# Kernel optimization log

Measured on AMD Instinct MI355X. Metric: run time of the kernel, lower is better.

The kernel has to match this reference:

```python
import jax, jax.numpy as jnp
import numpy as np

SH_C0 = 0.28209479177387814
SH_C1 = 0.4886025119029199
SH_C2 = (1.0925484305920792, -1.0925484305920792, 0.31539156525252005, -1.0925484305920792, 0.5462742152960396)
SH_C3 = (-0.5900435899266435, 2.890611442640554, -0.4570457994644658, 0.3731763325901154, -0.4570457994644658, 1.445305721320277, -0.5900435899266435)

BG = 128  # gaussians per compositing block


def quat_to_rot(q):
    # q: [N,4] normalized quaternion (w,x,y,z) -> [N,3,3]
    w, x, y, z = q[:, 0], q[:, 1], q[:, 2], q[:, 3]
    R = jnp.stack([
        1 - 2 * (y * y + z * z), 2 * (x * y - w * z), 2 * (x * z + w * y),
        2 * (x * y + w * z), 1 - 2 * (x * x + z * z), 2 * (y * z - w * x),
        2 * (x * z - w * y), 2 * (y * z + w * x), 1 - 2 * (x * x + y * y)],
        axis=-1)
    return R.reshape(-1, 3, 3)


def eval_sh(sh, d):
    # sh: [N,16,3] degree-3 SH coeffs; d: [N,3] unit view dirs -> [N,3] rgb
    x, y, z = d[:, 0:1], d[:, 1:2], d[:, 2:3]
    xx, yy, zz = x * x, y * y, z * z
    xy, yz, xz = x * y, y * z, x * z
    res = SH_C0 * sh[:, 0]
    res = res - SH_C1 * y * sh[:, 1] + SH_C1 * z * sh[:, 2] - SH_C1 * x * sh[:, 3]
    res = (res + SH_C2[0] * xy * sh[:, 4] + SH_C2[1] * yz * sh[:, 5]
           + SH_C2[2] * (2 * zz - xx - yy) * sh[:, 6]
           + SH_C2[3] * xz * sh[:, 7] + SH_C2[4] * (xx - yy) * sh[:, 8])
    res = (res + SH_C3[0] * y * (3 * xx - yy) * sh[:, 9] + SH_C3[1] * xy * z * sh[:, 10]
           + SH_C3[2] * y * (4 * zz - xx - yy) * sh[:, 11]
           + SH_C3[3] * z * (2 * zz - 3 * xx - 3 * yy) * sh[:, 12]
           + SH_C3[4] * x * (4 * zz - xx - yy) * sh[:, 13]
           + SH_C3[5] * z * (xx - yy) * sh[:, 14] + SH_C3[6] * x * (xx - 3 * yy) * sh[:, 15])
    return res


def gs_forward(pws, shs, alphas_raw, scales_raw, rots_raw, us, Rcw, tcw, intr, height, width):
    fx, fy, cx, cy = intr[0], intr[1], intr[2], intr[3]
    N = pws.shape[0]
    HW = height * width

    # activations (GSModel.forward)
    alphas = jax.nn.sigmoid(alphas_raw[:, 0])          # [N]
    scales = jnp.exp(scales_raw)                       # [N,3]
    rots = rots_raw / jnp.linalg.norm(rots_raw, axis=1, keepdims=True)

    # gsc.project
    pcs = pws @ Rcw.T + tcw                            # [N,3] camera frame
    depth = pcs[:, 2]
    zs = jnp.where(depth > 0.2, depth, 1.0)            # safe divide for culled pts
    u = jnp.stack([fx * pcs[:, 0] / zs + cx, fy * pcs[:, 1] / zs + cy], axis=-1)
    # the `us` input is a grad-capture dummy; forward value comes from projection
    u = u + us - jax.lax.stop_gradient(us)

    # gsc.computeCov3D: Cov3d = (R S)(R S)^T
    R = quat_to_rot(rots)
    M = R * scales[:, None, :]
    cov3d = M @ jnp.swapaxes(M, 1, 2)                  # [N,3,3]

    # gsc.computeCov2D: cov2d = J W Cov3d W^T J^T + 0.3 I
    tanfx = width / (2.0 * fx)
    tanfy = height / (2.0 * fy)
    tx = jnp.clip(pcs[:, 0] / zs, -1.3 * tanfx, 1.3 * tanfx) * zs
    ty = jnp.clip(pcs[:, 1] / zs, -1.3 * tanfy, 1.3 * tanfy) * zs
    zero = jnp.zeros_like(zs)
    J = jnp.stack([
        fx / zs, zero, -fx * tx / (zs * zs),
        zero, fy / zs, -fy * ty / (zs * zs)], axis=-1).reshape(N, 2, 3)
    T = jnp.einsum('nij,jk->nik', J, Rcw)              # [N,2,3]
    cov2d = jnp.einsum('nij,njk,nlk->nil', T, cov3d, T)
    cov2d = cov2d + 0.3 * jnp.eye(2, dtype=cov2d.dtype)
    a, b, c = cov2d[:, 0, 0], cov2d[:, 0, 1], cov2d[:, 1, 1]
    det = a * c - b * b
    valid = (depth > 0.2) & (det > 0)
    det_s = jnp.where(valid, det, 1.0)

    # gsc.inverseCov2D: conic + screen-space radius (areas)
    cinv = jnp.stack([c / det_s, -b / det_s, a / det_s], axis=-1)  # [N,3]
    mid = 0.5 * (a + c)
    lam = mid + jnp.sqrt(jnp.maximum(mid * mid - det, 0.1))
    radius = jnp.where(valid, jnp.ceil(3.0 * jnp.sqrt(lam)), 0.0)
    areas = jnp.stack([radius, radius], axis=-1)       # [N,2]

    # gsc.sh2Color
    twc = -Rcw.T @ tcw
    dirs = pws - twc
    dirs = dirs / jnp.linalg.norm(dirs, axis=1, keepdims=True)
    colors = jnp.maximum(eval_sh(shs.reshape(N, 16, 3), dirs) + 0.5, 0.0)  # [N,3]

    # gsc.splat: depth-sorted front-to-back alpha compositing over all pixels
    order = jnp.argsort(depth)
    nb = N // BG
    u_s = u[order].reshape(nb, BG, 2)
    cinv_s = cinv[order].reshape(nb, BG, 3)
    al_s = alphas[order].reshape(nb, BG)
    col_s = colors[order].reshape(nb, BG, 3)
    val_s = valid[order].reshape(nb, BG)

    ys, xs = jnp.meshgrid(jnp.arange(height, dtype=jnp.float32),
                          jnp.arange(width, dtype=jnp.float32), indexing='ij')
    px = xs.ravel()
    py = ys.ravel()

    @jax.checkpoint
    def body(carry, blk):
        logT, acc = carry                              # [HW], [3,HW]
        ub, cb, ab, colb, vb = blk
        dx = px[None, :] - ub[:, 0:1]                  # [BG,HW]
        dy = py[None, :] - ub[:, 1:2]
        power = -0.5 * (cb[:, 0:1] * dx * dx + cb[:, 2:3] * dy * dy) - cb[:, 1:2] * dx * dy
        alp = jnp.minimum(0.99, ab[:, None] * jnp.exp(power))
        alp = jnp.where((power <= 0) & (alp >= 1.0 / 255.0) & vb[:, None], alp, 0.0)
        l1m = jnp.log1p(-alp)
        cs = jnp.cumsum(l1m, axis=0)
        logT_i = logT[None, :] + jnp.concatenate(
            [jnp.zeros((1, HW), l1m.dtype), cs[:-1]], axis=0)  # exclusive transmittance
        Ti = jnp.exp(logT_i)
        w = jnp.where(Ti > 1e-4, alp * Ti, 0.0)        # early-termination at tau<1e-4
        acc = acc + jnp.einsum('gp,gc->cp', w, colb)
        return (logT + cs[-1], acc), None

    init = (jnp.zeros(HW, dtype=jnp.float32), jnp.zeros((3, HW), dtype=jnp.float32))
    (_, acc), _ = jax.lax.scan(body, init, (u_s, cinv_s, al_s, col_s, val_s))
    image = acc.reshape(3, height, width)
    return image, areas


def setup_inputs() -> dict:
    key = jax.random.key(0)
    ks = jax.random.split(key, 6)
    N, H, W = 8192, 256, 256
    pws = jax.random.normal(ks[0], (N, 3), jnp.float32) * 2.0 + jnp.array([0.0, 0.0, 6.0])
    shs = jax.random.normal(ks[1], (N, 48), jnp.float32) * 0.3
    alphas_raw = jax.random.normal(ks[2], (N, 1), jnp.float32)
    scales_raw = jax.random.normal(ks[3], (N, 3), jnp.float32) * 0.3 - 3.0
    rots_raw = jax.random.normal(ks[4], (N, 4), jnp.float32)
    us = jnp.zeros((N, 2), jnp.float32)
    Rcw = jnp.eye(3, dtype=jnp.float32)
    tcw = jnp.zeros((3,), jnp.float32)
    intr = jnp.array([400.0, 400.0, 128.0, 128.0], jnp.float32)  # fx, fy, cx, cy
    return {"pws": pws, "shs": shs, "alphas_raw": alphas_raw, "scales_raw": scales_raw,
            "rots_raw": rots_raw, "us": us, "Rcw": Rcw, "tcw": tcw, "intr": intr,
            "height": H, "width": W}


def reference(pws, shs, alphas_raw, scales_raw, rots_raw, us, Rcw, tcw, intr, height, width):
    return gs_forward(pws, shs, alphas_raw, scales_raw, rots_raw, us, Rcw, tcw, intr, height, width)
```

## Files before the change

### kernel.cpp

```cpp
#include <hip/hip_runtime.h>

__global__ __launch_bounds__(256) void k_pre(
    const float* __restrict__ pws, const float* __restrict__ shs,
    const float* __restrict__ alphas_raw, const float* __restrict__ scales_raw,
    const float* __restrict__ rots_raw, const float* __restrict__ Rcw,
    const float* __restrict__ tcw, const float* __restrict__ intr,
    int N, int W, int H, float* __restrict__ areas,
    unsigned long long* __restrict__ keys, unsigned* __restrict__ rank,
    float* __restrict__ P)
{
    int i = blockIdx.x * 256 + threadIdx.x;
    if (i >= N) return;
    rank[i] = 0u;

    float R00=Rcw[0],R01=Rcw[1],R02=Rcw[2];
    float R10=Rcw[3],R11=Rcw[4],R12=Rcw[5];
    float R20=Rcw[6],R21=Rcw[7],R22=Rcw[8];
    float t0=tcw[0],t1=tcw[1],t2=tcw[2];
    float fx=intr[0],fy=intr[1],cx=intr[2],cy=intr[3];

    float pwx=pws[i*3+0], pwy=pws[i*3+1], pwz=pws[i*3+2];
    float pcx = R00*pwx + R01*pwy + R02*pwz + t0;
    float pcy = R10*pwx + R11*pwy + R12*pwz + t1;
    float pcz = R20*pwx + R21*pwy + R22*pwz + t2;
    float depth = pcz;
    float zs = (depth > 0.2f) ? depth : 1.0f;
    float u0 = fx * pcx / zs + cx;
    float u1 = fy * pcy / zs + cy;

    float qw=rots_raw[i*4+0], qx=rots_raw[i*4+1], qy=rots_raw[i*4+2], qz=rots_raw[i*4+3];
    float qn = sqrtf(qw*qw + qx*qx + qy*qy + qz*qz);
    qw/=qn; qx/=qn; qy/=qn; qz/=qn;
    float s0 = expf(scales_raw[i*3+0]);
    float s1 = expf(scales_raw[i*3+1]);
    float s2 = expf(scales_raw[i*3+2]);

    float xx=qx*qx, yy=qy*qy, zq=qz*qz;
    float xy=qx*qy, xz=qx*qz, yz=qy*qz;
    float wx=qw*qx, wy=qw*qy, wz=qw*qz;
    float r00=1.f-2.f*(yy+zq), r01=2.f*(xy-wz),     r02=2.f*(xz+wy);
    float r10=2.f*(xy+wz),     r11=1.f-2.f*(xx+zq), r12=2.f*(yz-wx);
    float r20=2.f*(xz-wy),     r21=2.f*(yz+wx),     r22=1.f-2.f*(xx+yy);

    float m00=r00*s0, m01=r01*s1, m02=r02*s2;
    float m10=r10*s0, m11=r11*s1, m12=r12*s2;
    float m20=r20*s0, m21=r21*s1, m22=r22*s2;
    float V00=m00*m00+m01*m01+m02*m02;
    float V01=m00*m10+m01*m11+m02*m12;
    float V02=m00*m20+m01*m21+m02*m22;
    float V11=m10*m10+m11*m11+m12*m12;
    float V12=m10*m20+m11*m21+m12*m22;
    float V22=m20*m20+m21*m21+m22*m22;

    float tanfx = (float)W / (2.f*fx), tanfy = (float)H / (2.f*fy);
    float limx = 1.3f*tanfx, limy = 1.3f*tanfy;
    float txl = fminf(fmaxf(pcx/zs, -limx), limx) * zs;
    float tyl = fminf(fmaxf(pcy/zs, -limy), limy) * zs;
    float iz = 1.f/zs, iz2 = iz*iz;
    float J00 = fx*iz, J02 = -fx*txl*iz2;
    float J11 = fy*iz, J12 = -fy*tyl*iz2;

    float T00=J00*R00+J02*R20, T01=J00*R01+J02*R21, T02=J00*R02+J02*R22;
    float T10=J11*R10+J12*R20, T11=J11*R11+J12*R21, T12=J11*R12+J12*R22;
    float A0=T00*V00+T01*V01+T02*V02;
    float A1=T00*V01+T01*V11+T02*V12;
    float A2=T00*V02+T01*V12+T02*V22;
    float B0=T10*V00+T11*V01+T12*V02;
    float B1=T10*V01+T11*V11+T12*V12;
    float B2=T10*V02+T11*V12+T12*V22;
    float ca = A0*T00+A1*T01+A2*T02 + 0.3f;
    float cb = A0*T10+A1*T11+A2*T12;
    float cc = B0*T10+B1*T11+B2*T12 + 0.3f;

    float det = ca*cc - cb*cb;
    bool valid = (depth > 0.2f) && (det > 0.f);
    float det_s = valid ? det : 1.f;
    float dinv = 1.f/det_s;
    float ci0 =  cc*dinv, ci1 = -cb*dinv, ci2 = ca*dinv;
    float mid = 0.5f*(ca+cc);
    float lam = mid + sqrtf(fmaxf(mid*mid - det, 0.1f));
    float radius = valid ? ceilf(3.f*sqrtf(lam)) : 0.f;
    areas[2*i+0] = radius;
    areas[2*i+1] = radius;

    float alpha = 1.f/(1.f + expf(-alphas_raw[i]));

    float tw0 = -(R00*t0 + R10*t1 + R20*t2);
    float tw1 = -(R01*t0 + R11*t1 + R21*t2);
    float tw2 = -(R02*t0 + R12*t1 + R22*t2);
    float dx_=pwx-tw0, dy_=pwy-tw1, dz_=pwz-tw2;
    float dn = sqrtf(dx_*dx_+dy_*dy_+dz_*dz_);
    float x=dx_/dn, y=dy_/dn, z=dz_/dn;
    float sxx=x*x, syy=y*y, szz=z*z;
    float sxy=x*y, syz=y*z, sxz=x*z;
    const float* sh = shs + i*48;
    float col[3];
    #pragma unroll
    for (int c = 0; c < 3; ++c) {
        float res = 0.28209479177387814f*sh[0*3+c];
        res += -0.4886025119029199f*y*sh[1*3+c]
             +  0.4886025119029199f*z*sh[2*3+c]
             + -0.4886025119029199f*x*sh[3*3+c];
        res +=  1.0925484305920792f*sxy*sh[4*3+c]
             + -1.0925484305920792f*syz*sh[5*3+c]
             +  0.31539156525252005f*(2.f*szz-sxx-syy)*sh[6*3+c]
             + -1.0925484305920792f*sxz*sh[7*3+c]
             +  0.5462742152960396f*(sxx-syy)*sh[8*3+c];
        res += -0.5900435899266435f*y*(3.f*sxx-syy)*sh[9*3+c]
             +  2.890611442640554f*sxy*z*sh[10*3+c]
             + -0.4570457994644658f*y*(4.f*szz-sxx-syy)*sh[11*3+c]
             +  0.3731763325901154f*z*(2.f*szz-3.f*sxx-3.f*syy)*sh[12*3+c]
             + -0.4570457994644658f*x*(4.f*szz-sxx-syy)*sh[13*3+c]
             +  1.445305721320277f*z*(sxx-syy)*sh[14*3+c]
             + -0.5900435899266435f*x*(sxx-3.f*syy)*sh[15*3+c];
        col[c] = fmaxf(res + 0.5f, 0.f);
    }

    float rc2;
    if (!valid || 255.f*alpha < 0.999f) {
        rc2 = -1.f;
    } else {
        float r2 = 2.f*lam*logf(255.f*alpha);
        float r  = sqrtf(fmaxf(r2, 0.f)) + 1.f;
        rc2 = r*r;
    }

    P[0*N+i]=u0;  P[1*N+i]=u1;  P[2*N+i]=ci0; P[3*N+i]=ci1; P[4*N+i]=ci2;
    P[5*N+i]=alpha; P[6*N+i]=col[0]; P[7*N+i]=col[1]; P[8*N+i]=col[2];
    P[9*N+i]=rc2;

    unsigned ud = __float_as_uint(depth);
    ud = (ud & 0x80000000u) ? ~ud : (ud | 0x80000000u);
    keys[i] = ((unsigned long long)ud << 32) | (unsigned)i;
}

#define JC 512
__global__ __launch_bounds__(256) void k_rank(
    const unsigned long long* __restrict__ keys, int N,
    unsigned* __restrict__ rank)
{
    __shared__ unsigned long long sk[JC];
    const int j0 = blockIdx.y * JC;
    for (int t = threadIdx.x; t < JC; t += 256) {
        int j = j0 + t;
        sk[t] = (j < N) ? keys[j] : ~0ull;
    }
    __syncthreads();

    const int i0 = blockIdx.x * 512 + threadIdx.x;
    const int i1 = i0 + 256;
    unsigned long long my0 = (i0 < N) ? keys[i0] : 0ull;
    unsigned long long my1 = (i1 < N) ? keys[i1] : 0ull;

    int c0 = 0, c1 = 0;
    const ulonglong2* sk2 = (const ulonglong2*)sk;
    #pragma unroll 4
    for (int t = 0; t < JC/2; ++t) {
        ulonglong2 kk = sk2[t];
        c0 += (kk.x < my0) ? 1 : 0;
        c0 += (kk.y < my0) ? 1 : 0;
        c1 += (kk.x < my1) ? 1 : 0;
        c1 += (kk.y < my1) ? 1 : 0;
    }
    if (i0 < N) atomicAdd(&rank[i0], (unsigned)c0);
    if (i1 < N) atomicAdd(&rank[i1], (unsigned)c1);
}

__global__ __launch_bounds__(256) void k_scatter(
    const unsigned* __restrict__ rank, const float* __restrict__ Pun,
    float4* __restrict__ gA, float4* __restrict__ gB,
    float4* __restrict__ cull, int N)
{
    int i = blockIdx.x * 256 + threadIdx.x;
    if (i >= N) return;
    int s = (int)rank[i];
    cull[s] = make_float4(Pun[0*N+i], Pun[1*N+i], Pun[9*N+i], 0.f);
    gA[s]   = make_float4(Pun[2*N+i], Pun[3*N+i], Pun[4*N+i], Pun[5*N+i]);
    gB[s]   = make_float4(Pun[6*N+i], Pun[7*N+i], Pun[8*N+i], 0.f);
}

__global__ __launch_bounds__(256) void k_render(
    const float4* __restrict__ gA, const float4* __restrict__ gB,
    const float4* __restrict__ cull, int N, int W, int H,
    int nTiles, int nseg, float4* __restrict__ segbuf)
{
    const int tid = threadIdx.x;
    const int tilesX = (W + 15) >> 4;
    const int tile = blockIdx.x % nTiles, seg = blockIdx.x / nTiles;
    const int tX = tile % tilesX, tY = tile / tilesX;
    const int ix = (tX << 4) + (tid & 15);
    const int iy = (tY << 4) + (tid >> 4);
    const bool inb = (ix < W) && (iy < H);
    const float pxf = (float)ix, pyf = (float)iy;
    const float tx0 = (float)(tX << 4), ty0 = (float)(tY << 4);
    int tx1i = (tX << 4) + 15; if (tx1i > W-1) tx1i = W-1;
    int ty1i = (tY << 4) + 15; if (ty1i > H-1) ty1i = H-1;
    const float tx1 = (float)tx1i, ty1 = (float)ty1i;

    const int per = (N + nseg - 1) / nseg;
    const int g0 = seg * per;
    const int g1 = min(N, g0 + per);

    float T = inb ? 1.f : 0.f;
    float aR = 0.f, aG = 0.f, aB = 0.f;

    __shared__ float4 sG0[256];
    __shared__ float4 sG1[256];
    __shared__ float  sB2[256];
    __shared__ unsigned long long sMask[4];

    const int wave = tid >> 6, lane = tid & 63;

    for (int base = g0; base < g1; base += 256) {
        int g = base + tid;
        bool ov = false;
        float u0=0.f, u1=0.f;
        float4 a4 = make_float4(0.f,0.f,0.f,0.f);
        float4 b4 = make_float4(0.f,0.f,0.f,0.f);
        if (g < g1) {
            float4 cu = cull[g];
            u0 = cu.x; u1 = cu.y;
            float cxp = fminf(fmaxf(u0, tx0), tx1);
            float cyp = fminf(fmaxf(u1, ty0), ty1);
            float ddx = u0 - cxp, ddy = u1 - cyp;
            ov = (ddx*ddx + ddy*ddy) <= cu.z;
            if (ov) { a4 = gA[g]; b4 = gB[g]; }
        }
        unsigned long long m = __ballot(ov);
        if (lane == 0) sMask[wave] = m;
        __syncthreads();
        int cnt = 0, off = 0;
        #pragma unroll
        for (int w2 = 0; w2 < 4; ++w2) {
            int pc = __popcll(sMask[w2]);
            if (w2 < wave) off += pc;
            cnt += pc;
        }
        if (ov) {
            int pos = off + __popcll(m & ((1ull << lane) - 1ull));
            sG0[pos] = make_float4(u0, u1, a4.x, a4.y);
            sG1[pos] = make_float4(a4.z, a4.w, b4.x, b4.y);
            sB2[pos] = b4.z;
        }
        __syncthreads();

        for (int e = 0; e < cnt; ++e) {
            float4 e0 = sG0[e];
            float4 e1 = sG1[e];
            float  gb = sB2[e];
            float ddx = pxf - e0.x, ddy = pyf - e0.y;
            float power = -0.5f*(e0.z*ddx*ddx + e1.x*ddy*ddy) - e0.w*ddx*ddy;
            float alp = fminf(0.99f, e1.y * __expf(power));
            alp = (power <= 0.f && alp >= (1.0f/255.0f)) ? alp : 0.f;
            float w = (T > 0.0001f) ? alp * T : 0.f;
            aR = fmaf(w, e1.z, aR);
            aG = fmaf(w, e1.w, aG);
            aB = fmaf(w, gb, aB);
            T = T - T * alp;
        }
        int done = (T <= 0.0001f) ? 1 : 0;
        if (__syncthreads_and(done)) break;
    }

    if (inb) {
        int pix = iy * W + ix;
        segbuf[(size_t)seg * (size_t)(W*H) + pix] = make_float4(T, aR, aG, aB);
    }
}

__global__ __launch_bounds__(256) void k_combine(
    const float4* __restrict__ segbuf, int HW, int nseg,
    float* __restrict__ out)
{
    int p = blockIdx.x * 256 + threadIdx.x;
    if (p >= HW) return;
    float T = 1.f, r = 0.f, g = 0.f, b = 0.f;
    for (int s = 0; s < nseg; ++s) {
        float4 v = segbuf[(size_t)s * HW + p];
        r = fmaf(T, v.y, r);
        g = fmaf(T, v.z, g);
        b = fmaf(T, v.w, b);
        T *= v.x;
    }
    out[p] = r; out[HW + p] = g; out[2*HW + p] = b;
}

extern "C" void kernel_launch(void* const* d_in, const int* in_sizes, int n_in,
                              void* d_out, int out_size, void* d_ws, size_t ws_size,
                              hipStream_t stream) {
    const float* pws        = (const float*)d_in[0];
    const float* shs        = (const float*)d_in[1];
    const float* alphas_raw = (const float*)d_in[2];
    const float* scales_raw = (const float*)d_in[3];
    const float* rots_raw   = (const float*)d_in[4];
    const float* Rcw        = (const float*)d_in[6];
    const float* tcw        = (const float*)d_in[7];
    const float* intr       = (const float*)d_in[8];

    const int N  = in_sizes[0] / 3;
    const int HW = (out_size - 2 * N) / 3;
    int W = 1; while ((long long)W * W < (long long)HW) ++W;
    const int H = HW / W;

    float* out   = (float*)d_out;
    float* areas = out + 3 * HW;

    char* ws = (char*)d_ws;
    size_t off = 0;
    unsigned long long* keys = (unsigned long long*)(ws + off); off += (size_t)N * 8;
    unsigned* rank = (unsigned*)(ws + off);                     off += (size_t)N * 4;
    off = (off + 15) & ~(size_t)15;
    float* Pun = (float*)(ws + off);                            off += (size_t)10 * N * 4;
    off = (off + 15) & ~(size_t)15;
    float4* cullv = (float4*)(ws + off);                        off += (size_t)N * 16;
    float4* gA = (float4*)(ws + off);                           off += (size_t)N * 16;
    float4* gB = (float4*)(ws + off);                           off += (size_t)N * 16;
    float4* segbuf = (float4*)(ws + off);
    size_t remain = (ws_size > off) ? (ws_size - off) : 0;
    int nseg = 8;
    while (nseg > 1 && (size_t)nseg * (size_t)HW * 16 > remain) nseg >>= 1;

    int gsN = (N + 255) / 256;
    k_pre<<<gsN, 256, 0, stream>>>(pws, shs, alphas_raw, scales_raw, rots_raw,
                                   Rcw, tcw, intr, N, W, H, areas, keys, rank, Pun);
    dim3 rgrid((N + 511) / 512, (N + JC - 1) / JC);
    k_rank<<<rgrid, 256, 0, stream>>>(keys, N, rank);
    k_scatter<<<gsN, 256, 0, stream>>>(rank, Pun, gA, gB, cullv, N);
    int tilesX = (W + 15) / 16, tilesY = (H + 15) / 16;
    int nTiles = tilesX * tilesY;
    k_render<<<nTiles * nseg, 256, 0, stream>>>(gA, gB, cullv, N, W, H,
                                                nTiles, nseg, segbuf);
    k_combine<<<(HW + 255) / 256, 256, 0, stream>>>(segbuf, HW, nseg, out);
}
```

Measured before the change: 110.4 us.

## Fuse scatter into rank kernel and render tiles without depth segments

The rank kernel now packs a completion counter into the upper bits of each rank atomic. The last block to finish for a gaussian scatters its parameters directly, which removes the separate scatter launch. Rendering drops the depth-segment split and the combine kernel: each tile walks all gaussians front to back and writes the output directly, so the segment buffer traffic goes away. The cost is only 256 render blocks, fewer than before, so parallelism is lower and the early-exit on saturated transmittance has to make up for it.

```diff
diff --git a/kernel.cpp b/kernel.cpp
--- a/kernel.cpp
+++ b/kernel.cpp
@@ -135,12 +135,15 @@
 }
 
 #define JC 512
-__global__ __launch_bounds__(256) void k_rank(
+__global__ __launch_bounds__(256) void k_rank_scatter(
     const unsigned long long* __restrict__ keys, int N,
-    unsigned* __restrict__ rank)
+    unsigned* __restrict__ rank, const float* __restrict__ Pun,
+    float4* __restrict__ gA, float4* __restrict__ gB,
+    float4* __restrict__ cull)
 {
     __shared__ unsigned long long sk[JC];
     const int j0 = blockIdx.y * JC;
+    const int nJ = gridDim.y;
     for (int t = threadIdx.x; t < JC; t += 256) {
         int j = j0 + t;
         sk[t] = (j < N) ? keys[j] : ~0ull;
@@ -162,31 +165,34 @@
         c1 += (kk.x < my1) ? 1 : 0;
         c1 += (kk.y < my1) ? 1 : 0;
     }
-    if (i0 < N) atomicAdd(&rank[i0], (unsigned)c0);
-    if (i1 < N) atomicAdd(&rank[i1], (unsigned)c1);
-}
-
-__global__ __launch_bounds__(256) void k_scatter(
-    const unsigned* __restrict__ rank, const float* __restrict__ Pun,
-    float4* __restrict__ gA, float4* __restrict__ gB,
-    float4* __restrict__ cull, int N)
-{
-    int i = blockIdx.x * 256 + threadIdx.x;
-    if (i >= N) return;
-    int s = (int)rank[i];
-    cull[s] = make_float4(Pun[0*N+i], Pun[1*N+i], Pun[9*N+i], 0.f);
-    gA[s]   = make_float4(Pun[2*N+i], Pun[3*N+i], Pun[4*N+i], Pun[5*N+i]);
-    gB[s]   = make_float4(Pun[6*N+i], Pun[7*N+i], Pun[8*N+i], 0.f);
+    if (i0 < N) {
+        unsigned old = atomicAdd(&rank[i0], (unsigned)c0 + (1u << 20));
+        if ((int)(old >> 20) == nJ - 1) {
+            int s = (int)(old & 0xFFFFFu) + c0;
+            cull[s] = make_float4(Pun[0*N+i0], Pun[1*N+i0], Pun[9*N+i0], 0.f);
+            gA[s]   = make_float4(Pun[2*N+i0], Pun[3*N+i0], Pun[4*N+i0], Pun[5*N+i0]);
+            gB[s]   = make_float4(Pun[6*N+i0], Pun[7*N+i0], Pun[8*N+i0], 0.f);
+        }
+    }
+    if (i1 < N) {
+        unsigned old = atomicAdd(&rank[i1], (unsigned)c1 + (1u << 20));
+        if ((int)(old >> 20) == nJ - 1) {
+            int s = (int)(old & 0xFFFFFu) + c1;
+            cull[s] = make_float4(Pun[0*N+i1], Pun[1*N+i1], Pun[9*N+i1], 0.f);
+            gA[s]   = make_float4(Pun[2*N+i1], Pun[3*N+i1], Pun[4*N+i1], Pun[5*N+i1]);
+            gB[s]   = make_float4(Pun[6*N+i1], Pun[7*N+i1], Pun[8*N+i1], 0.f);
+        }
+    }
 }
 
 __global__ __launch_bounds__(256) void k_render(
     const float4* __restrict__ gA, const float4* __restrict__ gB,
     const float4* __restrict__ cull, int N, int W, int H,
-    int nTiles, int nseg, float4* __restrict__ segbuf)
+    float* __restrict__ out)
 {
     const int tid = threadIdx.x;
     const int tilesX = (W + 15) >> 4;
-    const int tile = blockIdx.x % nTiles, seg = blockIdx.x / nTiles;
+    const int tile = blockIdx.x;
     const int tX = tile % tilesX, tY = tile / tilesX;
     const int ix = (tX << 4) + (tid & 15);
     const int iy = (tY << 4) + (tid >> 4);
@@ -197,10 +203,6 @@
     int ty1i = (tY << 4) + 15; if (ty1i > H-1) ty1i = H-1;
     const float tx1 = (float)tx1i, ty1 = (float)ty1i;
 
-    const int per = (N + nseg - 1) / nseg;
-    const int g0 = seg * per;
-    const int g1 = min(N, g0 + per);
-
     float T = inb ? 1.f : 0.f;
     float aR = 0.f, aG = 0.f, aB = 0.f;
 
@@ -211,13 +213,13 @@
 
     const int wave = tid >> 6, lane = tid & 63;
 
-    for (int base = g0; base < g1; base += 256) {
+    for (int base = 0; base < N; base += 256) {
         int g = base + tid;
         bool ov = false;
         float u0=0.f, u1=0.f;
         float4 a4 = make_float4(0.f,0.f,0.f,0.f);
         float4 b4 = make_float4(0.f,0.f,0.f,0.f);
-        if (g < g1) {
+        if (g < N) {
             float4 cu = cull[g];
             u0 = cu.x; u1 = cu.y;
             float cxp = fminf(fmaxf(u0, tx0), tx1);
@@ -263,26 +265,12 @@
     }
 
     if (inb) {
+        int HW = W * H;
         int pix = iy * W + ix;
-        segbuf[(size_t)seg * (size_t)(W*H) + pix] = make_float4(T, aR, aG, aB);
-    }
-}
-
-__global__ __launch_bounds__(256) void k_combine(
-    const float4* __restrict__ segbuf, int HW, int nseg,
-    float* __restrict__ out)
-{
-    int p = blockIdx.x * 256 + threadIdx.x;
-    if (p >= HW) return;
-    float T = 1.f, r = 0.f, g = 0.f, b = 0.f;
-    for (int s = 0; s < nseg; ++s) {
-        float4 v = segbuf[(size_t)s * HW + p];
-        r = fmaf(T, v.y, r);
-        g = fmaf(T, v.z, g);
-        b = fmaf(T, v.w, b);
-        T *= v.x;
-    }
-    out[p] = r; out[HW + p] = g; out[2*HW + p] = b;
+        out[pix]        = aR;
+        out[HW + pix]   = aG;
+        out[2*HW + pix] = aB;
+    }
 }
 
 extern "C" void kernel_launch(void* const* d_in, const int* in_sizes, int n_in,
@@ -315,20 +303,13 @@
     float4* cullv = (float4*)(ws + off);                        off += (size_t)N * 16;
     float4* gA = (float4*)(ws + off);                           off += (size_t)N * 16;
     float4* gB = (float4*)(ws + off);                           off += (size_t)N * 16;
-    float4* segbuf = (float4*)(ws + off);
-    size_t remain = (ws_size > off) ? (ws_size - off) : 0;
-    int nseg = 8;
-    while (nseg > 1 && (size_t)nseg * (size_t)HW * 16 > remain) nseg >>= 1;
 
     int gsN = (N + 255) / 256;
     k_pre<<<gsN, 256, 0, stream>>>(pws, shs, alphas_raw, scales_raw, rots_raw,
                                    Rcw, tcw, intr, N, W, H, areas, keys, rank, Pun);
     dim3 rgrid((N + 511) / 512, (N + JC - 1) / JC);
-    k_rank<<<rgrid, 256, 0, stream>>>(keys, N, rank);
-    k_scatter<<<gsN, 256, 0, stream>>>(rank, Pun, gA, gB, cullv, N);
+    k_rank_scatter<<<rgrid, 256, 0, stream>>>(keys, N, rank, Pun, gA, gB, cullv);
     int tilesX = (W + 15) / 16, tilesY = (H + 15) / 16;
     int nTiles = tilesX * tilesY;
-    k_render<<<nTiles * nseg, 256, 0, stream>>>(gA, gB, cullv, N, W, H,
-                                                nTiles, nseg, segbuf);
-    k_combine<<<(HW + 255) / 256, 256, 0, stream>>>(segbuf, HW, nseg, out);
+    k_render<<<nTiles, 256, 0, stream>>>(gA, gB, cullv, N, W, H, out);
 }
```

Measured after the change: 129.3 us. 17.1% more time.
